# Optimization experiments

Measured on AMD Instinct MI355X. Metric: run time of the kernel, lower is better.

Reference implementation:

```python
import jax, jax.numpy as jnp
import numpy as np

MAX_NEIGHBORS = 64  # static cap; >> observed max (~50) for n=9225 uniform pts, r=0.03


def setup_inputs() -> dict:
    key = jax.random.key(0)
    k1, k2 = jax.random.split(key)
    n_batch, n, m, d = 8, 9225, 4096, 2
    data = jax.random.uniform(k1, (n_batch, n, d), dtype=jnp.float32)
    queries = jax.random.uniform(k2, (n_batch, m, d), dtype=jnp.float32)
    radius = jnp.float32(0.03)
    return {"data": data, "queries": queries, "radius": radius}


def reference(data, queries, radius):
    # Faithful JAX translation of native_neighbor_search (use_open3d=False),
    # computed in one shot instead of q_chunk loops (same math), with a static
    # neighbor cap MAX_NEIGHBORS standing in for the data-dependent max.
    B, n, d = data.shape
    m = queries.shape[1]
    # Squared Euclidean distances via the GEMM expansion (equiv. to cdist<=r).
    qn = jnp.sum(queries * queries, axis=-1)              # [B, m]
    dn = jnp.sum(data * data, axis=-1)                    # [B, n]
    cross = jnp.einsum("bmd,bnd->bmn", queries, data)    # [B, m, n]
    sqd = jnp.maximum(qn[:, :, None] + dn[:, None, :] - 2.0 * cross, 0.0)
    in_nbr = sqd <= radius * radius                       # [B, m, n] bool
    counts = jnp.sum(in_nbr, axis=2).astype(jnp.int32)    # [B, m]
    idx = jnp.arange(n, dtype=jnp.int32)                  # [n]
    # invalid slots -> sentinel n, sort compacts valid indices to the front
    valid = jnp.where(in_nbr, idx[None, None, :], jnp.int32(n))
    sorted_idx = jnp.sort(valid, axis=2)[:, :, :MAX_NEIGHBORS]
    neighbors_index = jnp.where(sorted_idx == n, jnp.int32(-1), sorted_idx)
    neighbors_row_splits = jnp.concatenate(
        [jnp.zeros((B, 1), dtype=jnp.int32), jnp.cumsum(counts, axis=1)], axis=1
    )
    return neighbors_index, neighbors_row_splits
```

## Files before the change

kernel.cpp:

```cpp
#include <hip/hip_runtime.h>

#define BATCH 8
#define NPTS 9225
#define MQ 4096
#define CAP 64
#define GRID 32
#define NCELLS (GRID * GRID)

__device__ __forceinline__ int cell_of(float x, float y) {
  int cx = (int)(x * (float)GRID);
  int cy = (int)(y * (float)GRID);
  cx = min(max(cx, 0), GRID - 1);
  cy = min(max(cy, 0), GRID - 1);
  return cy * GRID + cx;
}

__global__ __launch_bounds__(256) void zero_kernel(int* __restrict__ p, int n) {
  int i = blockIdx.x * blockDim.x + threadIdx.x;
  if (i < n) p[i] = 0;
}

__global__ __launch_bounds__(256) void hist_kernel(const float* __restrict__ data,
                                                   int* __restrict__ cell_counts) {
  int idx = blockIdx.x * blockDim.x + threadIdx.x;
  if (idx >= BATCH * NPTS) return;
  int b = idx / NPTS;
  const float2 p = ((const float2*)data)[idx];
  atomicAdd(&cell_counts[b * NCELLS + cell_of(p.x, p.y)], 1);
}

__global__ __launch_bounds__(1024) void cellscan_kernel(const int* __restrict__ cell_counts,
                                                        int* __restrict__ cell_starts,
                                                        int* __restrict__ cursors) {
  __shared__ int sc[NCELLS];
  const int b = blockIdx.x;
  const int t = threadIdx.x;
  const int v = cell_counts[b * NCELLS + t];
  sc[t] = v;
  __syncthreads();
  for (int off = 1; off < NCELLS; off <<= 1) {
    int u = (t >= off) ? sc[t - off] : 0;
    __syncthreads();
    sc[t] += u;
    __syncthreads();
  }
  const int incl = sc[t];
  const int excl = incl - v;
  cell_starts[b * (NCELLS + 1) + t] = excl;
  cursors[b * NCELLS + t] = excl;
  if (t == NCELLS - 1) cell_starts[b * (NCELLS + 1) + NCELLS] = incl;
}

__global__ __launch_bounds__(256) void scatter_kernel(const float* __restrict__ data,
                                                      int* __restrict__ cursors,
                                                      float2* __restrict__ sdata,
                                                      int* __restrict__ sidx) {
  int idx = blockIdx.x * blockDim.x + threadIdx.x;
  if (idx >= BATCH * NPTS) return;
  int b = idx / NPTS;
  int i = idx - b * NPTS;
  const float2 p = ((const float2*)data)[idx];
  int pos = atomicAdd(&cursors[b * NCELLS + cell_of(p.x, p.y)], 1);
  sdata[b * NPTS + pos] = p;
  sidx[b * NPTS + pos] = i;
}

__global__ __launch_bounds__(256) void search_kernel(
    const float* __restrict__ queries, const float* __restrict__ radius_p,
    const int* __restrict__ cell_starts, const float2* __restrict__ sdata,
    const int* __restrict__ sidx, int* __restrict__ nbr_idx,
    int* __restrict__ counts) {
#pragma clang fp contract(off)
  __shared__ int hitbuf[4][CAP];
  const int wave_g = (blockIdx.x * blockDim.x + threadIdx.x) >> 6;
  const int lane = threadIdx.x & 63;
  const int w = (threadIdx.x >> 6) & 3;
  if (wave_g >= BATCH * MQ) return;
  const int q = wave_g;
  const int b = q >> 12;
  const float r = radius_p[0];
  const float r2 = r * r;
  const float2 qv = ((const float2*)queries)[q];
  const float qx = qv.x, qy = qv.y;
  const float qn = qx * qx + qy * qy;

  int cx = min(max((int)(qx * (float)GRID), 0), GRID - 1);
  int cy = min(max((int)(qy * (float)GRID), 0), GRID - 1);
  const int x0 = max(cx - 1, 0), x1 = min(cx + 1, GRID - 1);
  const int y0 = max(cy - 1, 0), y1 = min(cy + 1, GRID - 1);

  const unsigned long long below = (1ull << lane) - 1ull;
  const int csbase = b * (NCELLS + 1);
  const float2* sd = sdata + b * NPTS;
  const int* si = sidx + b * NPTS;
  int h = 0;

  for (int y = y0; y <= y1; ++y) {
    const int s0 = cell_starts[csbase + y * GRID + x0];
    const int s1 = cell_starts[csbase + y * GRID + x1 + 1];
    for (int off = s0; off < s1; off += 64) {
      const int i = off + lane;
      const bool act = (i < s1);
      float dx = 0.f, dy = 0.f;
      int id = 0;
      if (act) {
        const float2 p = sd[i];
        dx = p.x; dy = p.y;
        id = si[i];
      }
      const float dn = dx * dx + dy * dy;
      const float cross = qx * dx + qy * dy;
      const float s = (qn + dn) - 2.0f * cross;
      const bool in = act && (s <= r2);
      const unsigned long long mask = __ballot(in);
      if (in) {
        const int pos = h + __popcll(mask & below);
        if (pos < CAP) hitbuf[w][pos] = id;
      }
      h += __popcll(mask);
    }
  }

  int v = (lane < h && lane < CAP) ? hitbuf[w][lane] : 0x7fffffff;

#pragma unroll
  for (int k = 2; k <= 64; k <<= 1) {
#pragma unroll
    for (int j = k >> 1; j >= 1; j >>= 1) {
      const int other = __shfl_xor(v, j, 64);
      const bool up = ((lane & k) == 0);
      const bool lower = ((lane & j) == 0);
      const bool keep_min = (up == lower);
      v = keep_min ? min(v, other) : max(v, other);
    }
  }

  nbr_idx[(size_t)q * CAP + lane] = (v == 0x7fffffff) ? -1 : v;
  if (lane == 0) counts[q] = h;
}

__global__ __launch_bounds__(256) void scan_kernel(const int* __restrict__ counts,
                                                   int* __restrict__ row_splits) {
  const int b = blockIdx.x;
  const int t = threadIdx.x;
  const int T = 256;
  const int PER = MQ / T;
  __shared__ int partial[T];
  const int* c = counts + b * MQ;
  int local[PER];
  int sum = 0;
#pragma unroll
  for (int k = 0; k < PER; ++k) { local[k] = c[t * PER + k]; sum += local[k]; }
  partial[t] = sum;
  __syncthreads();
  for (int off = 1; off < T; off <<= 1) {
    int v = (t >= off) ? partial[t - off] : 0;
    __syncthreads();
    partial[t] += v;
    __syncthreads();
  }
  const int excl = (t == 0) ? 0 : partial[t - 1];
  int* rs = row_splits + b * (MQ + 1);
  if (t == 0) rs[0] = 0;
  int run = excl;
#pragma unroll
  for (int k = 0; k < PER; ++k) { run += local[k]; rs[t * PER + k + 1] = run; }
}

extern "C" void kernel_launch(void* const* d_in, const int* in_sizes, int n_in,
                              void* d_out, int out_size, void* d_ws, size_t ws_size,
                              hipStream_t stream) {
  const float* data    = (const float*)d_in[0];
  const float* queries = (const float*)d_in[1];
  const float* radius  = (const float*)d_in[2];
  int* out        = (int*)d_out;
  int* nbr_idx    = out;
  int* row_splits = out + BATCH * MQ * CAP;

  int* counts      = (int*)d_ws;
  int* cell_counts = counts + BATCH * MQ;
  int* cell_starts = cell_counts + BATCH * NCELLS;
  int* cursors     = cell_starts + BATCH * (NCELLS + 1);
  int* sidx        = cursors + BATCH * NCELLS;
  float2* sdata    = (float2*)(sidx + BATCH * NPTS);

  const int npts_blocks = (BATCH * NPTS + 255) / 256;
  hipLaunchKernelGGL(zero_kernel, dim3((BATCH * NCELLS + 255) / 256), dim3(256), 0, stream,
                     cell_counts, BATCH * NCELLS);
  hipLaunchKernelGGL(hist_kernel, dim3(npts_blocks), dim3(256), 0, stream,
                     data, cell_counts);
  hipLaunchKernelGGL(cellscan_kernel, dim3(BATCH), dim3(NCELLS), 0, stream,
                     cell_counts, cell_starts, cursors);
  hipLaunchKernelGGL(scatter_kernel, dim3(npts_blocks), dim3(256), 0, stream,
                     data, cursors, sdata, sidx);
  hipLaunchKernelGGL(search_kernel, dim3(BATCH * MQ / 4), dim3(256), 0, stream,
                     queries, radius, cell_starts, sdata, sidx, nbr_idx, counts);
  hipLaunchKernelGGL(scan_kernel, dim3(BATCH), dim3(256), 0, stream,
                     counts, row_splits);
}
```

Before: 92.98 us.

## Fuse grid build into one per-batch kernel and flatten search loop

Result: slower. 102.9 us (+10.7%).

```diff
diff --git a/kernel.cpp b/kernel.cpp
--- a/kernel.cpp
+++ b/kernel.cpp
@@ -15,54 +15,52 @@
   return cy * GRID + cx;
 }
 
-__global__ __launch_bounds__(256) void zero_kernel(int* __restrict__ p, int n) {
-  int i = blockIdx.x * blockDim.x + threadIdx.x;
-  if (i < n) p[i] = 0;
-}
-
-__global__ __launch_bounds__(256) void hist_kernel(const float* __restrict__ data,
-                                                   int* __restrict__ cell_counts) {
-  int idx = blockIdx.x * blockDim.x + threadIdx.x;
-  if (idx >= BATCH * NPTS) return;
-  int b = idx / NPTS;
-  const float2 p = ((const float2*)data)[idx];
-  atomicAdd(&cell_counts[b * NCELLS + cell_of(p.x, p.y)], 1);
-}
-
-__global__ __launch_bounds__(1024) void cellscan_kernel(const int* __restrict__ cell_counts,
-                                                        int* __restrict__ cell_starts,
-                                                        int* __restrict__ cursors) {
-  __shared__ int sc[NCELLS];
+__global__ __launch_bounds__(1024) void build_kernel(
+    const float* __restrict__ data,
+    int* __restrict__ cell_starts,
+    float2* __restrict__ sdata, int* __restrict__ sidx) {
+  __shared__ int hist[NCELLS];
+  __shared__ int cursor[NCELLS];
   const int b = blockIdx.x;
   const int t = threadIdx.x;
-  const int v = cell_counts[b * NCELLS + t];
-  sc[t] = v;
-  __syncthreads();
+  hist[t] = 0;
+  __syncthreads();
+
+  const float2* dp = (const float2*)data + (size_t)b * NPTS;
+  float2 pts[10];
+  int cells[10];
+  int np = 0;
+  for (int i = t; i < NPTS; i += 1024) {
+    const float2 p = dp[i];
+    const int c = cell_of(p.x, p.y);
+    pts[np] = p;
+    cells[np] = c;
+    ++np;
+    atomicAdd(&hist[c], 1);
+  }
+  __syncthreads();
+
+  const int v = hist[t];
   for (int off = 1; off < NCELLS; off <<= 1) {
-    int u = (t >= off) ? sc[t - off] : 0;
-    __syncthreads();
-    sc[t] += u;
-    __syncthreads();
-  }
-  const int incl = sc[t];
+    const int u = (t >= off) ? hist[t - off] : 0;
+    __syncthreads();
+    hist[t] += u;
+    __syncthreads();
+  }
+  const int incl = hist[t];
   const int excl = incl - v;
+  cursor[t] = excl;
   cell_starts[b * (NCELLS + 1) + t] = excl;
-  cursors[b * NCELLS + t] = excl;
   if (t == NCELLS - 1) cell_starts[b * (NCELLS + 1) + NCELLS] = incl;
-}
-
-__global__ __launch_bounds__(256) void scatter_kernel(const float* __restrict__ data,
-                                                      int* __restrict__ cursors,
-                                                      float2* __restrict__ sdata,
-                                                      int* __restrict__ sidx) {
-  int idx = blockIdx.x * blockDim.x + threadIdx.x;
-  if (idx >= BATCH * NPTS) return;
-  int b = idx / NPTS;
-  int i = idx - b * NPTS;
-  const float2 p = ((const float2*)data)[idx];
-  int pos = atomicAdd(&cursors[b * NCELLS + cell_of(p.x, p.y)], 1);
-  sdata[b * NPTS + pos] = p;
-  sidx[b * NPTS + pos] = i;
+  __syncthreads();
+
+  float2* sd = sdata + (size_t)b * NPTS;
+  int* si = sidx + (size_t)b * NPTS;
+  for (int k = 0; k < np; ++k) {
+    const int pos = atomicAdd(&cursor[cells[k]], 1);
+    sd[pos] = pts[k];
+    si[pos] = t + k * 1024;
+  }
 }
 
 __global__ __launch_bounds__(256) void search_kernel(
@@ -84,35 +82,48 @@
   const float qx = qv.x, qy = qv.y;
   const float qn = qx * qx + qy * qy;
 
-  int cx = min(max((int)(qx * (float)GRID), 0), GRID - 1);
-  int cy = min(max((int)(qy * (float)GRID), 0), GRID - 1);
+  const int cx = min(max((int)(qx * (float)GRID), 0), GRID - 1);
+  const int cy = min(max((int)(qy * (float)GRID), 0), GRID - 1);
   const int x0 = max(cx - 1, 0), x1 = min(cx + 1, GRID - 1);
   const int y0 = max(cy - 1, 0), y1 = min(cy + 1, GRID - 1);
 
-  const unsigned long long below = (1ull << lane) - 1ull;
   const int csbase = b * (NCELLS + 1);
-  const float2* sd = sdata + b * NPTS;
-  const int* si = sidx + b * NPTS;
-  int h = 0;
-
+  int rstart[3], rlen[3];
+  int nr = 0;
   for (int y = y0; y <= y1; ++y) {
     const int s0 = cell_starts[csbase + y * GRID + x0];
     const int s1 = cell_starts[csbase + y * GRID + x1 + 1];
-    for (int off = s0; off < s1; off += 64) {
-      const int i = off + lane;
-      const bool act = (i < s1);
-      float dx = 0.f, dy = 0.f;
-      int id = 0;
-      if (act) {
-        const float2 p = sd[i];
-        dx = p.x; dy = p.y;
-        id = si[i];
-      }
-      const float dn = dx * dx + dy * dy;
-      const float cross = qx * dx + qy * dy;
-      const float s = (qn + dn) - 2.0f * cross;
-      const bool in = act && (s <= r2);
-      const unsigned long long mask = __ballot(in);
+    rstart[nr] = s0;
+    rlen[nr] = s1 - s0;
+    ++nr;
+  }
+  for (int k = nr; k < 3; ++k) { rstart[k] = 0; rlen[k] = 0; }
+  const int L0 = rlen[0];
+  const int L01 = L0 + rlen[1];
+  const int T = L01 + rlen[2];
+
+  const unsigned long long below = (1ull << lane) - 1ull;
+  const float2* sd = sdata + (size_t)b * NPTS;
+  const int* si = sidx + (size_t)b * NPTS;
+  int h = 0;
+
+  for (int base = 0; base < T; base += 64) {
+    const int p = base + lane;
+    const bool act = (p < T);
+    int i;
+    if (p < L0)        i = rstart[0] + p;
+    else if (p < L01)  i = rstart[1] + (p - L0);
+    else               i = rstart[2] + (p - L01);
+    if (!act) i = 0;
+    const float2 pt = sd[i];
+    const int id = si[i];
+    const float dx = pt.x, dy = pt.y;
+    const float dn = dx * dx + dy * dy;
+    const float cross = qx * dx + qy * dy;
+    const float s = (qn + dn) - 2.0f * cross;
+    const bool in = act && (s <= r2);
+    const unsigned long long mask = __ballot(in);
+    if (mask != 0ull) {
       if (in) {
         const int pos = h + __popcll(mask & below);
         if (pos < CAP) hitbuf[w][pos] = id;
@@ -124,13 +135,19 @@
   int v = (lane < h && lane < CAP) ? hitbuf[w][lane] : 0x7fffffff;
 
 #pragma unroll
-  for (int k = 2; k <= 64; k <<= 1) {
+  for (int k = 2; k <= 32; k <<= 1) {
 #pragma unroll
     for (int j = k >> 1; j >= 1; j >>= 1) {
       const int other = __shfl_xor(v, j, 64);
-      const bool up = ((lane & k) == 0);
-      const bool lower = ((lane & j) == 0);
-      const bool keep_min = (up == lower);
+      const bool keep_min = (((lane & k) == 0) == ((lane & j) == 0));
+      v = keep_min ? min(v, other) : max(v, other);
+    }
+  }
+  if (h > 32) {
+#pragma unroll
+    for (int j = 32; j >= 1; j >>= 1) {
+      const int other = __shfl_xor(v, j, 64);
+      const bool keep_min = ((lane & j) == 0);
       v = keep_min ? min(v, other) : max(v, other);
     }
   }
@@ -154,9 +171,9 @@
   partial[t] = sum;
   __syncthreads();
   for (int off = 1; off < T; off <<= 1) {
-    int v = (t >= off) ? partial[t - off] : 0;
-    __syncthreads();
-    partial[t] += v;
+    int u = (t >= off) ? partial[t - off] : 0;
+    __syncthreads();
+    partial[t] += u;
     __syncthreads();
   }
   const int excl = (t == 0) ? 0 : partial[t - 1];
@@ -178,21 +195,12 @@
   int* row_splits = out + BATCH * MQ * CAP;
 
   int* counts      = (int*)d_ws;
-  int* cell_counts = counts + BATCH * MQ;
-  int* cell_starts = cell_counts + BATCH * NCELLS;
-  int* cursors     = cell_starts + BATCH * (NCELLS + 1);
-  int* sidx        = cursors + BATCH * NCELLS;
+  int* cell_starts = counts + BATCH * MQ;
+  int* sidx        = cell_starts + BATCH * (NCELLS + 1);
   float2* sdata    = (float2*)(sidx + BATCH * NPTS);
 
-  const int npts_blocks = (BATCH * NPTS + 255) / 256;
-  hipLaunchKernelGGL(zero_kernel, dim3((BATCH * NCELLS + 255) / 256), dim3(256), 0, stream,
-                     cell_counts, BATCH * NCELLS);
-  hipLaunchKernelGGL(hist_kernel, dim3(npts_blocks), dim3(256), 0, stream,
-                     data, cell_counts);
-  hipLaunchKernelGGL(cellscan_kernel, dim3(BATCH), dim3(NCELLS), 0, stream,
-                     cell_counts, cell_starts, cursors);
-  hipLaunchKernelGGL(scatter_kernel, dim3(npts_blocks), dim3(256), 0, stream,
-                     data, cursors, sdata, sidx);
+  hipLaunchKernelGGL(build_kernel, dim3(BATCH), dim3(1024), 0, stream,
+                     data, cell_starts, sdata, sidx);
   hipLaunchKernelGGL(search_kernel, dim3(BATCH * MQ / 4), dim3(256), 0, stream,
                      queries, radius, cell_starts, sdata, sidx, nbr_idx, counts);
   hipLaunchKernelGGL(scan_kernel, dim3(BATCH), dim3(256), 0, stream,
```
